# Performance work log

Hardware: AMD Instinct MI355X
Metric: run time of the kernel (lower is better)

The kernel has to match this reference:

```python
import jax, jax.numpy as jnp
import numpy as np
import math

B, T, D, DI, DFF, H = 4, 1024, 1024, 256, 4096, 16
S, N, E = 16, 256, 1024          # stat_num, token_num, exemplar_len
STAT_K, TOKEN_K = 8, 16
NEG = -1e6


def setup_inputs() -> dict:
    key = jax.random.key(0)
    ks = jax.random.split(key, 32)
    r = lambda i, shape: jax.random.normal(ks[i], shape, jnp.float32)
    w = lambda i, shape: r(i, shape) * 0.02
    return dict(
        x=r(0, (B, T, D)),
        stat_enc=r(1, (B * S, N, D)),
        exemplar_enc=r(2, (B, E, D)),
        stat_feature=r(3, (B, S, D)),
        intent_embed=r(4, (B, 1, DI)),
        Wq1=w(5, (D, D)), Wk1=w(6, (D, D)), Wv1=w(7, (D, D)), Wo1=w(8, (D, D)),
        Wq_stat=w(9, (D + DI, D)), Wq_token=w(10, (D + DI, D)),
        Wk_stat=w(11, (D, D)), Wk_token=w(12, (D, D)),
        Wv_sel=w(13, (D, D)), Wo_sel=w(14, (D, D)),
        Wq2=w(15, (D + DI, D)), Wk2=w(16, (D, D)), Wv2=w(17, (D, D)), Wo2=w(18, (D, D)),
        Wg=w(19, (2 * D, 1)),
        W1=w(20, (D, DFF)), b1=jnp.zeros((DFF,), jnp.float32),
        W2=w(21, (DFF, D)), b2=jnp.zeros((D,), jnp.float32),
        g1=jnp.ones((D,), jnp.float32), be1=jnp.zeros((D,), jnp.float32),
        g2=jnp.ones((D,), jnp.float32), be2=jnp.zeros((D,), jnp.float32),
        g3=jnp.ones((D,), jnp.float32), be3=jnp.zeros((D,), jnp.float32),
        stat_valid_len=jax.random.randint(ks[22], (B,), 1, S + 1),
        example_valid_len=jax.random.randint(ks[23], (B,), 1, E + 1),
    )


def _ln(x, g, b):
    m = x.mean(-1, keepdims=True)
    v = ((x - m) ** 2).mean(-1, keepdims=True)
    return (x - m) / jnp.sqrt(v + 1e-5) * g + b


def _mha(q, k, v, valid, Wq, Wk, Wv, Wo):
    Bq, Tq, _ = q.shape
    Sk = k.shape[1]
    sp = lambda z: z.reshape(Bq, z.shape[1], H, -1).transpose(0, 2, 1, 3)  # B,H,L,dh
    qh, kh, vh = sp(q @ Wq), sp(k @ Wk), sp(v @ Wv)
    dh = qh.shape[-1]
    sc = jnp.einsum('bhtd,bhsd->bhts', qh, kh) / math.sqrt(dh)
    vl = valid[:, None, None, None] if valid.ndim == 1 else valid[:, None, :, None]
    sc = jnp.where(jnp.arange(Sk)[None, None, None, :] < vl, sc, NEG)
    w = jax.nn.softmax(sc, axis=-1)
    out = jnp.einsum('bhts,bhsd->bhtd', w, vh).transpose(0, 2, 1, 3).reshape(Bq, Tq, -1)
    return out @ Wo


def _scatter_topk(scores, k):
    # keep top-k per row, everything else -> NEG (matches torch topk+scatter)
    shp = scores.shape
    flat = scores.reshape(-1, shp[-1])
    vals, idx = jax.lax.top_k(flat, k)
    out = jnp.full_like(flat, NEG).at[jnp.arange(flat.shape[0])[:, None], idx].set(vals)
    return out.reshape(shp)


def reference(x, stat_enc, exemplar_enc, stat_feature, intent_embed,
              Wq1, Wk1, Wv1, Wo1,
              Wq_stat, Wq_token, Wk_stat, Wk_token, Wv_sel, Wo_sel,
              Wq2, Wk2, Wv2, Wo2, Wg,
              W1, b1, W2, b2,
              g1, be1, g2, be2, g3, be3,
              stat_valid_len, example_valid_len):
    # masked self-attention (training mode -> causal valid lens)
    dec_valid = jnp.broadcast_to(jnp.arange(1, T + 1)[None, :], (B, T))
    x2 = _mha(x, x, x, dec_valid, Wq1, Wk1, Wv1, Wo1)
    y = _ln(x + x2, g1, be1)
    yi = jnp.concatenate([y, jnp.broadcast_to(intent_embed, (B, T, DI))], axis=-1)

    # selective hierarchical top-k attention
    qs = yi @ Wq_stat                      # [B,T,D]
    qt = yi @ Wq_token                     # [B,T,D]
    ks = stat_feature @ Wk_stat            # [B,S,D]
    kt = (stat_enc @ Wk_token).reshape(B, S, N, D)
    vv = (stat_enc @ Wv_sel).reshape(B, S, N, D)
    scale = math.sqrt(D)
    ssc = jnp.einsum('btd,bsd->bts', qs, ks) / scale
    ssc = jnp.where(jnp.arange(S)[None, None, :] < stat_valid_len[:, None, None], ssc, NEG)
    sw = jax.nn.softmax(_scatter_topk(ssc, min(S - 1, STAT_K)), axis=-1)   # [B,T,S]
    tsc = jnp.einsum('btd,bsnd->btsn', qt, kt) / scale                      # [B,T,S,N]
    tw = jax.nn.softmax(_scatter_topk(tsc, min(N - 1, TOKEN_K)), axis=-1)
    comb = sw[..., None] * tw                                               # [B,T,S,N]
    y2s = jnp.einsum('btsn,bsnd->btd', comb, vv) @ Wo_sel

    # exemplar cross-attention
    y2e = _mha(yi, exemplar_enc, exemplar_enc, example_valid_len, Wq2, Wk2, Wv2, Wo2)

    gate = jax.nn.sigmoid(jnp.concatenate([y2s, y2e], axis=-1) @ Wg)
    y2 = gate * y2s + (1.0 - gate) * y2e
    z = _ln(y + 2.0 * y2, g2, be2)
    ffn = jax.nn.relu(z @ W1 + b1) @ W2 + b2
    return _ln(z + ffn, g3, be3)
```

## Files before the change

kernel.cpp:

```cpp
#include <hip/hip_runtime.h>

typedef unsigned short u16;
typedef short s16x8 __attribute__((ext_vector_type(8)));
typedef u16 u16x4 __attribute__((ext_vector_type(4)));
typedef float f32x4 __attribute__((ext_vector_type(4)));

#define T_N   1024
#define NEGV  -1e6f
#define MB    (1L << 20)

__device__ __forceinline__ u16 f2bf(float f) {
    unsigned u = __float_as_uint(f);
    u += 0x7fffu + ((u >> 16) & 1u);
    return (u16)(u >> 16);
}
__device__ __forceinline__ float bf2f(u16 h) {
    return __uint_as_float(((unsigned)h) << 16);
}
__device__ __forceinline__ f32x4 mfma16(s16x8 a, s16x8 b, f32x4 c) {
    return __builtin_amdgcn_mfma_f32_16x16x32_bf16(a, b, c, 0, 0, 0);
}
__device__ __forceinline__ void gll16(const u16* g, u16* l) {
    __builtin_amdgcn_global_load_lds((const __attribute__((address_space(1))) void*)g,
                                     (__attribute__((address_space(3))) void*)l, 16, 0, 0);
}

struct P6 { const float* s[6]; u16* d[6]; };

__global__ __launch_bounds__(256) void transpose_cast_batch(P6 pp, int K, int N) {
    const float* __restrict__ src = pp.s[blockIdx.z];
    u16* __restrict__ dst = pp.d[blockIdx.z];
    __shared__ float tile[32][33];
    int nb = blockIdx.x * 32, kb = blockIdx.y * 32;
    int tx = threadIdx.x & 31, ty = threadIdx.x >> 5;
    #pragma unroll
    for (int i = 0; i < 4; i++)
        tile[ty + 8*i][tx] = src[(long)(kb + ty + 8*i) * N + nb + tx];
    __syncthreads();
    #pragma unroll
    for (int i = 0; i < 4; i++)
        dst[(long)(nb + ty + 8*i) * K + kb + tx] = f2bf(tile[tx][ty + 8*i]);
}

__global__ __launch_bounds__(256) void cast_bf16_kernel(const float* __restrict__ src,
                                                        u16* __restrict__ dst, long n) {
    long i = ((long)blockIdx.x * 256 + threadIdx.x) * 4;
    if (i >= n) return;
    float4 v = *(const float4*)(src + i);
    u16x4 o = { f2bf(v.x), f2bf(v.y), f2bf(v.z), f2bf(v.w) };
    *(u16x4*)(dst + i) = o;
}

template<typename OutT, bool RELU, bool HAS_BIAS>
__global__ __launch_bounds__(256) void gemm_bt(
    const u16* __restrict__ A, const u16* __restrict__ Bt, OutT* __restrict__ C,
    const float* __restrict__ bias, int M, int N, int K,
    int lda, int ldb, int ldc,
    int batchDivA, long sA, long sB, long sC)
{
    A  += (long)(blockIdx.z / batchDivA) * sA;
    Bt += (long)blockIdx.z * sB;
    C  += (long)blockIdx.z * sC;
    __shared__ __align__(16) u16 As[4096];
    __shared__ __align__(16) u16 Bs[4096];
    const int tid = threadIdx.x;
    const int wave = tid >> 6, lane = tid & 63;
    const int quad = lane >> 4, l16 = lane & 15;
    const int wr = (wave >> 1) * 64, wc = (wave & 1) * 64;
    const long row0 = (long)blockIdx.y * 128, col0 = (long)blockIdx.x * 128;

    f32x4 acc[4][4] = {};

    const int l4r = lane >> 2;
    const int l4c = (lane & 3) * 8;
    const int ra = wave * 32 + l4r;
    const u16* Ap0 = A + (row0 + ra) * (long)lda + l4c;
    const u16* Ap1 = Ap0 + 16L * lda;
    const u16* Bp0 = Bt + (col0 + ra) * (long)ldb + l4c;
    const u16* Bp1 = Bp0 + 16L * ldb;
    u16* AsW0 = &As[(wave * 32) * 32];
    u16* AsW1 = &As[(wave * 32 + 16) * 32];
    u16* BsW0 = &Bs[(wave * 32) * 32];
    u16* BsW1 = &Bs[(wave * 32 + 16) * 32];
    const bool aok0 = (row0 + wave * 32) < M;
    const bool aok1 = (row0 + wave * 32 + 16) < M;

    for (int k0 = 0; k0 < K; k0 += 32) {
        __syncthreads();
        if (aok0) gll16(Ap0 + k0, AsW0);
        if (aok1) gll16(Ap1 + k0, AsW1);
        gll16(Bp0 + k0, BsW0);
        gll16(Bp1 + k0, BsW1);
        __syncthreads();
        s16x8 af[4], bfr[4];
        #pragma unroll
        for (int i = 0; i < 4; i++)
            af[i]  = *(const s16x8*)&As[(wr + i*16 + l16) * 32 + quad*8];
        #pragma unroll
        for (int j = 0; j < 4; j++)
            bfr[j] = *(const s16x8*)&Bs[(wc + j*16 + l16) * 32 + quad*8];
        #pragma unroll
        for (int i = 0; i < 4; i++)
            #pragma unroll
            for (int j = 0; j < 4; j++)
                acc[i][j] = mfma16(af[i], bfr[j], acc[i][j]);
    }

    #pragma unroll
    for (int i = 0; i < 4; i++) {
        long row = row0 + wr + i*16 + quad*4;
        #pragma unroll
        for (int j = 0; j < 4; j++) {
            long col = col0 + wc + j*16 + l16;
            float bv = 0.f;
            if constexpr (HAS_BIAS) bv = bias[col];
            #pragma unroll
            for (int r = 0; r < 4; r++) {
                if (row + r < M) {
                    float v = acc[i][j][r] + bv;
                    if constexpr (RELU) v = fmaxf(v, 0.f);
                    if constexpr (sizeof(OutT) == 2) C[(row + r) * (long)ldc + col] = f2bf(v);
                    else                             C[(row + r) * (long)ldc + col] = v;
                }
            }
        }
    }
}

template<typename OutT, bool RELU, bool HAS_BIAS>
__global__ __launch_bounds__(512, 2) void gemm_bt256(
    const u16* __restrict__ A, const u16* __restrict__ Bt, OutT* __restrict__ C,
    const float* __restrict__ bias, int M, int N, int K,
    int lda, int ldb, int ldc,
    int batchDivA, long sA, long sB, long sC)
{
    A  += (long)(blockIdx.z / batchDivA) * sA;
    Bt += (long)blockIdx.z * sB;
    C  += (long)blockIdx.z * sC;
    __shared__ __align__(16) u16 As[4][8192];
    __shared__ __align__(16) u16 Bs[4][8192];
    const int tid = threadIdx.x;
    const int wave = tid >> 6, lane = tid & 63;
    const int quad = lane >> 4, l16 = lane & 15;
    const int wm = wave >> 2, wn = wave & 3;
    const long row0 = (long)blockIdx.y * 256, col0 = (long)blockIdx.x * 256;

    const int srow = tid >> 2;
    const int scol = ((tid & 3) ^ ((srow >> 1) & 3)) * 8;
    const u16* Ag = A  + (row0 + srow) * (long)lda + scol;
    const u16* Bg = Bt + (col0 + srow) * (long)ldb + scol;
    const int ldsoff = wave * 512;

    f32x4 acc[8][4] = {};
    const int NT = K >> 5;

    auto stageA = [&](int kt, int buf) {
        gll16(Ag + (long)kt * 32,            &As[buf][ldsoff]);
        gll16(Ag + (long)kt * 32 + 128L*lda, &As[buf][4096 + ldsoff]);
    };
    auto stageB = [&](int kt, int buf) {
        gll16(Bg + (long)kt * 32,            &Bs[buf][ldsoff]);
        gll16(Bg + (long)kt * 32 + 128L*ldb, &Bs[buf][4096 + ldsoff]);
    };

    stageA(0, 0); stageB(0, 0);
    stageA(1, 1); stageB(1, 1);
    stageA(2, 2); stageB(2, 2);
    asm volatile("s_waitcnt vmcnt(8)" ::: "memory");
    __builtin_amdgcn_s_barrier();

    const int arow = wm * 128 + l16;
    const int brow = wn * 64  + l16;
    const int kq   = (quad ^ ((l16 >> 1) & 3)) * 8;

    for (int kt = 0; kt < NT; ++kt) {
        const int b  = kt & 3;
        const int sb = (kt + 3) & 3;
        const bool st = (kt + 3) < NT;
        const u16* Ab = As[b];
        const u16* Bb = Bs[b];

        s16x8 bfr[4], af[4];
        #pragma unroll
        for (int j = 0; j < 4; ++j)
            bfr[j] = *(const s16x8*)&Bb[(brow + j*16) * 32 + kq];
        #pragma unroll
        for (int i = 0; i < 4; ++i)
            af[i] = *(const s16x8*)&Ab[(arow + i*16) * 32 + kq];
        if (st) stageA(kt + 3, sb);
        __builtin_amdgcn_s_barrier();
        asm volatile("s_waitcnt lgkmcnt(0)" ::: "memory");
        __builtin_amdgcn_sched_barrier(0);
        __builtin_amdgcn_s_setprio(1);
        #pragma unroll
        for (int i = 0; i < 4; ++i)
            #pragma unroll
            for (int j = 0; j < 4; ++j)
                acc[i][j] = mfma16(af[i], bfr[j], acc[i][j]);
        __builtin_amdgcn_s_setprio(0);
        __builtin_amdgcn_s_barrier();

        #pragma unroll
        for (int i = 0; i < 4; ++i)
            af[i] = *(const s16x8*)&Ab[(arow + (i + 4)*16) * 32 + kq];
        if (st) stageB(kt + 3, sb);
        __builtin_amdgcn_s_barrier();
        asm volatile("s_waitcnt lgkmcnt(0)" ::: "memory");
        __builtin_amdgcn_sched_barrier(0);
        __builtin_amdgcn_s_setprio(1);
        #pragma unroll
        for (int i = 0; i < 4; ++i)
            #pragma unroll
            for (int j = 0; j < 4; ++j)
                acc[i + 4][j] = mfma16(af[i], bfr[j], acc[i + 4][j]);
        __builtin_amdgcn_s_setprio(0);

        const int rem = NT - 2 - kt;
        if (rem >= 2)      asm volatile("s_waitcnt vmcnt(8)" ::: "memory");
        else if (rem == 1) asm volatile("s_waitcnt vmcnt(4)" ::: "memory");
        else if (rem == 0) asm volatile("s_waitcnt vmcnt(0)" ::: "memory");
        __builtin_amdgcn_s_barrier();
    }

    #pragma unroll
    for (int i = 0; i < 8; ++i) {
        const long row = row0 + wm*128 + i*16 + quad*4;
        #pragma unroll
        for (int j = 0; j < 4; ++j) {
            const long col = col0 + wn*64 + j*16 + l16;
            float bv = 0.f;
            if constexpr (HAS_BIAS) bv = bias[col];
            #pragma unroll
            for (int r = 0; r < 4; ++r) {
                float v = acc[i][j][r] + bv;
                if constexpr (RELU) v = fmaxf(v, 0.f);
                if constexpr (sizeof(OutT) == 2) C[(row + r) * (long)ldc + col] = f2bf(v);
                else                             C[(row + r) * (long)ldc + col] = v;
            }
        }
    }
}

template<bool CAUSAL>
__global__ __launch_bounds__(256) void flash_attn_kernel(
    const u16* __restrict__ Q, const u16* __restrict__ Kg, const u16* __restrict__ Vg,
    const int* __restrict__ valid_len, u16* __restrict__ O,
    int qld, int kld, int vld)
{
    const int h = blockIdx.y, b = blockIdx.z;
    const int qt0 = blockIdx.x * 64;
    const int tid = threadIdx.x;
    const int wave = tid >> 6, lane = tid & 63;
    const int quad = lane >> 4, l16 = lane & 15;

    __shared__ __align__(16) u16 Qs[64][72];
    __shared__ __align__(16) u16 Ks[64][72];
    __shared__ __align__(16) u16 Vt[64][72];
    __shared__ __align__(16) u16 Ps[4][16][72];

    const int sr = tid >> 2, scc = (tid & 3) * 16;
    {
        const u16* qp = Q + ((long)b * T_N + qt0 + sr) * qld + h * 64 + scc;
        *(s16x8*)&Qs[sr][scc]     = *(const s16x8*)qp;
        *(s16x8*)&Qs[sr][scc + 8] = *(const s16x8*)(qp + 8);
    }
    float m_i[4] = {-1e30f, -1e30f, -1e30f, -1e30f};
    float l_i[4] = {0.f, 0.f, 0.f, 0.f};
    f32x4 o_acc[4] = {};

    int vl = 0, kend;
    if (CAUSAL) kend = qt0 + 64;
    else { vl = valid_len[b]; kend = (vl + 63) & ~63; }

    for (int kv0 = 0; kv0 < kend; kv0 += 64) {
        __syncthreads();
        {
            const u16* kp = Kg + ((long)b * T_N + kv0 + sr) * kld + h * 64 + scc;
            *(s16x8*)&Ks[sr][scc]     = *(const s16x8*)kp;
            *(s16x8*)&Ks[sr][scc + 8] = *(const s16x8*)(kp + 8);
            const u16* vp = Vg + ((long)b * T_N + kv0 + sr) * vld + h * 64 + scc;
            s16x8 v0 = *(const s16x8*)vp;
            s16x8 v1 = *(const s16x8*)(vp + 8);
            #pragma unroll
            for (int j = 0; j < 8; j++) {
                Vt[scc + j][sr]     = (u16)v0[j];
                Vt[scc + 8 + j][sr] = (u16)v1[j];
            }
        }
        __syncthreads();
        f32x4 sc[4] = {};
        #pragma unroll
        for (int kk = 0; kk < 64; kk += 32) {
            s16x8 aq = *(const s16x8*)&Qs[wave*16 + l16][kk + quad*8];
            #pragma unroll
            for (int j = 0; j < 4; j++) {
                s16x8 bk = *(const s16x8*)&Ks[j*16 + l16][kk + quad*8];
                sc[j] = mfma16(aq, bk, sc[j]);
            }
        }
        const int qrow = qt0 + wave*16 + quad*4;
        #pragma unroll
        for (int j = 0; j < 4; j++) {
            int kcol = kv0 + j*16 + l16;
            #pragma unroll
            for (int r = 0; r < 4; r++) {
                float s = sc[j][r] * 0.125f;
                bool ok = CAUSAL ? (kcol <= qrow + r) : (kcol < vl);
                sc[j][r] = ok ? s : -1e30f;
            }
        }
        float alpha[4];
        #pragma unroll
        for (int r = 0; r < 4; r++) {
            float mx = fmaxf(fmaxf(sc[0][r], sc[1][r]), fmaxf(sc[2][r], sc[3][r]));
            #pragma unroll
            for (int d = 1; d < 16; d <<= 1) mx = fmaxf(mx, __shfl_xor(mx, d, 64));
            float mn = fmaxf(m_i[r], mx);
            alpha[r] = __expf(m_i[r] - mn);
            m_i[r] = mn;
        }
        float rsum[4] = {0.f, 0.f, 0.f, 0.f};
        #pragma unroll
        for (int j = 0; j < 4; j++)
            #pragma unroll
            for (int r = 0; r < 4; r++) {
                float pv = __expf(sc[j][r] - m_i[r]);
                sc[j][r] = pv;
                rsum[r] += pv;
            }
        #pragma unroll
        for (int r = 0; r < 4; r++) {
            #pragma unroll
            for (int d = 1; d < 16; d <<= 1) rsum[r] += __shfl_xor(rsum[r], d, 64);
            l_i[r] = l_i[r] * alpha[r] + rsum[r];
        }
        #pragma unroll
        for (int j = 0; j < 4; j++)
            #pragma unroll
            for (int r = 0; r < 4; r++)
                Ps[wave][quad*4 + r][j*16 + l16] = f2bf(sc[j][r]);
        #pragma unroll
        for (int j2 = 0; j2 < 4; j2++)
            #pragma unroll
            for (int r = 0; r < 4; r++)
                o_acc[j2][r] *= alpha[r];
        __syncthreads();
        #pragma unroll
        for (int kk = 0; kk < 64; kk += 32) {
            s16x8 ap = *(const s16x8*)&Ps[wave][l16][kk + quad*8];
            #pragma unroll
            for (int j2 = 0; j2 < 4; j2++) {
                s16x8 bv = *(const s16x8*)&Vt[j2*16 + l16][kk + quad*8];
                o_acc[j2] = mfma16(ap, bv, o_acc[j2]);
            }
        }
    }
    #pragma unroll
    for (int j2 = 0; j2 < 4; j2++) {
        #pragma unroll
        for (int r = 0; r < 4; r++) {
            float v = o_acc[j2][r] / l_i[r];
            long row = (long)b * T_N + qt0 + wave*16 + quad*4 + r;
            O[row * 1024 + h*64 + j2*16 + l16] = f2bf(v);
        }
    }
}

__global__ __launch_bounds__(256) void ssc_kernel(
    const u16* __restrict__ qs, const u16* __restrict__ ks,
    const int* __restrict__ svl, float* __restrict__ ssc, int qld)
{
    const int t = blockIdx.x, b = blockIdx.y;
    const int wave = threadIdx.x >> 6, lane = threadIdx.x & 63;
    const u16* qrow = qs + ((long)b * T_N + t) * qld + lane * 16;
    const int vl = svl[b];
    for (int s = wave; s < 16; s += 4) {
        const u16* krow = ks + ((long)b * 16 + s) * 1024 + lane * 16;
        float acc = 0.f;
        #pragma unroll
        for (int seg = 0; seg < 2; seg++) {
            s16x8 qv = *(const s16x8*)(qrow + seg*8);
            s16x8 kv = *(const s16x8*)(krow + seg*8);
            #pragma unroll
            for (int j = 0; j < 8; j++) acc += bf2f((u16)qv[j]) * bf2f((u16)kv[j]);
        }
        #pragma unroll
        for (int d = 1; d < 64; d <<= 1) acc += __shfl_xor(acc, d, 64);
        if (lane == 0)
            ssc[((long)b * T_N + t) * 16 + s] = (s < vl) ? acc * (1.f/32.f) : NEGV;
    }
}

__global__ __launch_bounds__(256) void select_combine_kernel(
    const float* __restrict__ ssc, const float* __restrict__ tsc,
    const u16* __restrict__ vv, u16* __restrict__ out, int t0, int vld)
{
    const int tl = blockIdx.x, b = blockIdx.y;
    const int tg = t0 + tl;
    const int tid = threadIdx.x;
    const int wave = tid >> 6, lane = tid & 63;
    __shared__ float coeff[128];
    __shared__ long  rowoff[128];
    __shared__ int   sel_s[8];
    __shared__ float sel_w[8];

    if (wave == 0) {
        float cur = (lane < 16) ? ssc[((long)b * T_N + tg) * 16 + lane] : -3e38f;
        float mx0 = 0.f, ssum = 0.f, myv = -3e38f;
        int myi = 0;
        #pragma unroll
        for (int it = 0; it < 8; it++) {
            float mv = cur; int mi = lane;
            #pragma unroll
            for (int d = 1; d < 64; d <<= 1) {
                float ov = __shfl_xor(mv, d, 64);
                int   oi = __shfl_xor(mi, d, 64);
                if (ov > mv || (ov == mv && oi < mi)) { mv = ov; mi = oi; }
            }
            if (it == 0) mx0 = mv;
            ssum += __expf(mv - mx0);
            if (lane == it) { myv = mv; myi = mi; }
            if (lane == mi) cur = -3e38f;
        }
        if (lane < 8) { sel_s[lane] = myi; sel_w[lane] = __expf(myv - mx0) / ssum; }
    }
    __syncthreads();

    for (int slot = wave; slot < 8; slot += 4) {
        int s = sel_s[slot];
        float sw = sel_w[slot];
        const float* trow = tsc + (((long)b * 16 + s) * 512 + tl) * 256;
        float4 lv4 = *(const float4*)(trow + lane * 4);
        float loc[4] = { lv4.x, lv4.y, lv4.z, lv4.w };
        float mx0 = 0.f, tsum = 0.f, myv = -3e38f;
        int myi = 0;
        for (int it = 0; it < 16; it++) {
            float mv = -3e38f; int mi = 0;
            #pragma unroll
            for (int u = 0; u < 4; u++)
                if (loc[u] > mv) { mv = loc[u]; mi = lane*4 + u; }
            #pragma unroll
            for (int d = 1; d < 64; d <<= 1) {
                float ov = __shfl_xor(mv, d, 64);
                int   oi = __shfl_xor(mi, d, 64);
                if (ov > mv || (ov == mv && oi < mi)) { mv = ov; mi = oi; }
            }
            if (it == 0) mx0 = mv * (1.f/32.f);
            tsum += __expf(mv * (1.f/32.f) - mx0);
            if (lane == it) { myv = mv; myi = mi; }
            if ((mi >> 2) == lane) {
                int u = mi & 3;
                if (u == 0) loc[0] = -3e38f;
                else if (u == 1) loc[1] = -3e38f;
                else if (u == 2) loc[2] = -3e38f;
                else loc[3] = -3e38f;
            }
        }
        if (lane < 16) {
            coeff[slot * 16 + lane]  = sw * __expf(myv * (1.f/32.f) - mx0) / tsum;
            rowoff[slot * 16 + lane] = (long)((b * 16 + s) * 256 + myi) * vld;
        }
    }
    __syncthreads();

    const int d0 = tid * 4;
    float a0 = 0.f, a1 = 0.f, a2 = 0.f, a3 = 0.f;
    for (int r = 0; r < 128; r++) {
        float c = coeff[r];
        const u16* vp = vv + rowoff[r] + d0;
        u16x4 v4 = *(const u16x4*)vp;
        a0 += c * bf2f(v4[0]);
        a1 += c * bf2f(v4[1]);
        a2 += c * bf2f(v4[2]);
        a3 += c * bf2f(v4[3]);
    }
    u16x4 o4 = { f2bf(a0), f2bf(a1), f2bf(a2), f2bf(a3) };
    *(u16x4*)(out + ((long)b * T_N + tg) * 1024 + d0) = o4;
}

__device__ __forceinline__ float block_sum(float v, float* red) {
    #pragma unroll
    for (int d = 1; d < 64; d <<= 1) v += __shfl_xor(v, d, 64);
    __syncthreads();
    if ((threadIdx.x & 63) == 0) red[threadIdx.x >> 6] = v;
    __syncthreads();
    return red[0] + red[1] + red[2] + red[3];
}

__global__ __launch_bounds__(256) void ln1_kernel(
    const float* __restrict__ x, const float* __restrict__ x2,
    const float* __restrict__ intent, const float* __restrict__ g, const float* __restrict__ be,
    u16* __restrict__ yi)
{
    __shared__ float red[4];
    const long row = blockIdx.x;
    const int tid = threadIdx.x;
    const long base = row * 1024 + tid * 4;
    float4 xv = *(const float4*)(x + base);
    float4 dv = *(const float4*)(x2 + base);
    float h0 = xv.x + dv.x, h1 = xv.y + dv.y, h2 = xv.z + dv.z, h3 = xv.w + dv.w;
    float s1 = block_sum(h0 + h1 + h2 + h3, red);
    float s2 = block_sum(h0*h0 + h1*h1 + h2*h2 + h3*h3, red);
    float mean = s1 * (1.f/1024.f);
    float var = s2 * (1.f/1024.f) - mean * mean;
    float inv = rsqrtf(var + 1e-5f);
    const int c = tid * 4;
    float4 gv = *(const float4*)(g + c);
    float4 bv = *(const float4*)(be + c);
    float o0 = (h0 - mean) * inv * gv.x + bv.x;
    float o1 = (h1 - mean) * inv * gv.y + bv.y;
    float o2 = (h2 - mean) * inv * gv.z + bv.z;
    float o3 = (h3 - mean) * inv * gv.w + bv.w;
    u16x4 ob = { f2bf(o0), f2bf(o1), f2bf(o2), f2bf(o3) };
    *(u16x4*)(yi + row * 1280 + c) = ob;
    const int b = (int)(row >> 10);
    yi[row * 1280 + 1024 + tid] = f2bf(intent[b * 256 + tid]);
}

__global__ __launch_bounds__(256) void gate_ln2_kernel(
    const u16* __restrict__ yi, const float* __restrict__ y2s, const float* __restrict__ y2e,
    const float* __restrict__ Wg, const float* __restrict__ g, const float* __restrict__ be,
    float* __restrict__ z, u16* __restrict__ zbf)
{
    __shared__ float red[4];
    const long row = blockIdx.x;
    const int tid = threadIdx.x;
    const long base = row * 1024 + tid * 4;
    const int c = tid * 4;
    float4 sv = *(const float4*)(y2s + base);
    float4 ev = *(const float4*)(y2e + base);
    float4 w1 = *(const float4*)(Wg + c);
    float4 w2 = *(const float4*)(Wg + 1024 + c);
    float dot = sv.x*w1.x + sv.y*w1.y + sv.z*w1.z + sv.w*w1.w
              + ev.x*w2.x + ev.y*w2.y + ev.z*w2.z + ev.w*w2.w;
    float tot = block_sum(dot, red);
    float gate = 1.f / (1.f + __expf(-tot));
    u16x4 yv4 = *(const u16x4*)(yi + row * 1280 + c);
    float h0 = bf2f(yv4[0]) + 2.f * (gate * sv.x + (1.f - gate) * ev.x);
    float h1 = bf2f(yv4[1]) + 2.f * (gate * sv.y + (1.f - gate) * ev.y);
    float h2 = bf2f(yv4[2]) + 2.f * (gate * sv.z + (1.f - gate) * ev.z);
    float h3 = bf2f(yv4[3]) + 2.f * (gate * sv.w + (1.f - gate) * ev.w);
    float s1 = block_sum(h0 + h1 + h2 + h3, red);
    float s2 = block_sum(h0*h0 + h1*h1 + h2*h2 + h3*h3, red);
    float mean = s1 * (1.f/1024.f);
    float var = s2 * (1.f/1024.f) - mean * mean;
    float inv = rsqrtf(var + 1e-5f);
    float4 gv = *(const float4*)(g + c);
    float4 bv = *(const float4*)(be + c);
    float o0 = (h0 - mean) * inv * gv.x + bv.x;
    float o1 = (h1 - mean) * inv * gv.y + bv.y;
    float o2 = (h2 - mean) * inv * gv.z + bv.z;
    float o3 = (h3 - mean) * inv * gv.w + bv.w;
    *(float4*)(z + base) = make_float4(o0, o1, o2, o3);
    u16x4 ob = { f2bf(o0), f2bf(o1), f2bf(o2), f2bf(o3) };
    *(u16x4*)(zbf + row * 1024 + c) = ob;
}

__global__ __launch_bounds__(256) void ln3_kernel(
    const float* __restrict__ z, const float* __restrict__ p0, const float* __restrict__ p1,
    const float* __restrict__ b2,
    const float* __restrict__ g, const float* __restrict__ be, float* __restrict__ out)
{
    __shared__ float red[4];
    const long row = blockIdx.x;
    const int tid = threadIdx.x;
    const long base = row * 1024 + tid * 4;
    const int c = tid * 4;
    float4 zv = *(const float4*)(z + base);
    float4 f0 = *(const float4*)(p0 + base);
    float4 f1 = *(const float4*)(p1 + base);
    float4 bb = *(const float4*)(b2 + c);
    float h0 = zv.x + f0.x + f1.x + bb.x;
    float h1 = zv.y + f0.y + f1.y + bb.y;
    float h2 = zv.z + f0.z + f1.z + bb.z;
    float h3 = zv.w + f0.w + f1.w + bb.w;
    float s1 = block_sum(h0 + h1 + h2 + h3, red);
    float s2 = block_sum(h0*h0 + h1*h1 + h2*h2 + h3*h3, red);
    float mean = s1 * (1.f/1024.f);
    float var = s2 * (1.f/1024.f) - mean * mean;
    float inv = rsqrtf(var + 1e-5f);
    float4 gv = *(const float4*)(g + c);
    float4 bv = *(const float4*)(be + c);
    float o0 = (h0 - mean) * inv * gv.x + bv.x;
    float o1 = (h1 - mean) * inv * gv.y + bv.y;
    float o2 = (h2 - mean) * inv * gv.z + bv.z;
    float o3 = (h3 - mean) * inv * gv.w + bv.w;
    *(float4*)(out + base) = make_float4(o0, o1, o2, o3);
}

extern "C" void kernel_launch(void* const* d_in, const int* in_sizes, int n_in,
                              void* d_out, int out_size, void* d_ws, size_t ws_size,
                              hipStream_t stream)
{
    (void)in_sizes; (void)n_in; (void)out_size; (void)ws_size;
    const float* x      = (const float*)d_in[0];
    const float* stat_e = (const float*)d_in[1];
    const float* exem   = (const float*)d_in[2];
    const float* sfeat  = (const float*)d_in[3];
    const float* intent = (const float*)d_in[4];
    const float* Wg  = (const float*)d_in[19];
    const float* b1  = (const float*)d_in[21];
    const float* b2  = (const float*)d_in[23];
    const float* g1  = (const float*)d_in[24]; const float* be1 = (const float*)d_in[25];
    const float* g2  = (const float*)d_in[26]; const float* be2 = (const float*)d_in[27];
    const float* g3  = (const float*)d_in[28]; const float* be3 = (const float*)d_in[29];
    const int* svl = (const int*)d_in[30];
    const int* evl = (const int*)d_in[31];
    float* outp = (float*)d_out;

    char* base = (char*)d_ws;
    u16*  bufA  = (u16*)(base + 0*MB);
    u16*  qkv1  = (u16*)(base + 8*MB);
    float* x2a  = (float*)(base + 8*MB);
    u16*  kv2   = (u16*)(base + 8*MB);
    u16*  w1t   = (u16*)(base + 8*MB);
    u16*  w2t   = (u16*)(base + 16*MB);
    u16*  yibf  = (u16*)(base + 32*MB);
    u16*  buf3  = (u16*)(base + 42*MB);
    u16*  zbf   = (u16*)(base + 42*MB);
    u16*  sebf  = (u16*)(base + 66*MB);
    float* tsch = (float*)(base + 66*MB);
    u16*  hid   = (u16*)(base + 66*MB);
    u16*  ktvv  = (u16*)(base + 98*MB);
    float* y2sf = (float*)(base + 98*MB);
    float* p0f  = (float*)(base + 98*MB);
    u16*  exbf  = (u16*)(base + 114*MB);
    float* y2ef = (float*)(base + 122*MB);
    float* zf   = (float*)(base + 138*MB);
    u16*  sfbf  = (u16*)(base + 162*MB);
    u16*  ksbf  = (u16*)(base + 162*MB + 256*1024);
    float* sscf = (float*)(base + 162*MB + 512*1024);
    char* wpool = base + 163*MB;

    dim3 blk(256);
    dim3 blk512(512);
    auto cast = [&](const float* s, u16* d, long n) {
        cast_bf16_kernel<<<dim3((unsigned)((n/4 + 255) / 256)), blk, 0, stream>>>(s, d, n);
    };
    auto g_n = [&](const u16* A, const u16* Bt, u16* C, int M, int N, int K,
                   int lda, int ldb, int ldc) {
        gemm_bt<u16,false,false><<<dim3(N/128, (M+127)/128, 1), blk, 0, stream>>>(
            A, Bt, C, nullptr, M, N, K, lda, ldb, ldc, 1, 0, 0, 0);
    };
    auto g_f = [&](const u16* A, const u16* Bt, float* C, int M, int N, int K,
                   int lda, int ldb, int ldc) {
        gemm_bt<float,false,false><<<dim3(N/128, (M+127)/128, 1), blk, 0, stream>>>(
            A, Bt, C, nullptr, M, N, K, lda, ldb, ldc, 1, 0, 0, 0);
    };
    auto g256_n = [&](const u16* A, const u16* Bt, u16* C, int M, int N, int K,
                      int lda, int ldb, int ldc) {
        gemm_bt256<u16,false,false><<<dim3(N/256, M/256, 1), blk512, 0, stream>>>(
            A, Bt, C, nullptr, M, N, K, lda, ldb, ldc, 1, 0, 0, 0);
    };

    u16* wqkv1t = (u16*)wpool;
    u16* wo1t   = (u16*)(wpool) + 3L*1024*1024;
    {
        P6 pp{};
        pp.s[0]=(const float*)d_in[5]; pp.d[0]=wqkv1t;
        pp.s[1]=(const float*)d_in[6]; pp.d[1]=wqkv1t + 1L*1024*1024;
        pp.s[2]=(const float*)d_in[7]; pp.d[2]=wqkv1t + 2L*1024*1024;
        pp.s[3]=(const float*)d_in[8]; pp.d[3]=wo1t;
        transpose_cast_batch<<<dim3(32, 32, 4), blk, 0, stream>>>(pp, 1024, 1024);
    }
    cast(x, bufA, 4096L*1024);
    g256_n(bufA, wqkv1t, qkv1, 4096, 3072, 1024, 1024, 1024, 3072);
    flash_attn_kernel<true><<<dim3(16, 16, 4), blk, 0, stream>>>(
        qkv1, qkv1 + 1024, qkv1 + 2048, nullptr, bufA, 3072, 3072, 3072);
    g_f(bufA, wo1t, x2a, 4096, 1024, 1024, 1024, 1024, 1024);
    ln1_kernel<<<dim3(4096), blk, 0, stream>>>(x, x2a, intent, g1, be1, yibf);

    u16* wq3t = (u16*)wpool;
    {
        P6 pp{};
        pp.s[0]=(const float*)d_in[9];  pp.d[0]=wq3t;
        pp.s[1]=(const float*)d_in[10]; pp.d[1]=wq3t + 1L*1024*1280;
        pp.s[2]=(const float*)d_in[15]; pp.d[2]=wq3t + 2L*1024*1280;
        transpose_cast_batch<<<dim3(32, 40, 3), blk, 0, stream>>>(pp, 1280, 1024);
    }
    g256_n(yibf, wq3t, buf3, 4096, 3072, 1280, 1280, 1280, 3072);
    u16* wkst = (u16*)wpool;
    u16* wkv  = (u16*)(wpool) + 1L*1024*1024;
    {
        P6 pp{};
        pp.s[0]=(const float*)d_in[11]; pp.d[0]=wkst;
        pp.s[1]=(const float*)d_in[12]; pp.d[1]=wkv;
        pp.s[2]=(const float*)d_in[13]; pp.d[2]=wkv + 1L*1024*1024;
        transpose_cast_batch<<<dim3(32, 32, 3), blk, 0, stream>>>(pp, 1024, 1024);
    }
    cast(sfeat, sfbf, 64L*1024);
    cast(stat_e, sebf, 16384L*1024);
    g_n(sfbf, wkst, ksbf, 64, 1024, 1024, 1024, 1024, 1024);
    g256_n(sebf, wkv, ktvv, 16384, 2048, 1024, 1024, 1024, 2048);
    ssc_kernel<<<dim3(1024, 4), blk, 0, stream>>>(buf3, ksbf, svl, sscf, 3072);
    for (int hh = 0; hh < 2; hh++) {
        long t0 = hh * 512;
        gemm_bt<float,false,false><<<dim3(2, 4, 64), blk, 0, stream>>>(
            buf3 + 1024 + t0*3072, ktvv, tsch, nullptr, 512, 256, 1024,
            3072, 2048, 256, 16, (long)T_N*3072, 256L*2048, 512L*256);
        select_combine_kernel<<<dim3(512, 4), blk, 0, stream>>>(
            sscf, tsch, ktvv + 1024, bufA, (int)t0, 2048);
    }
    u16* wost = (u16*)wpool;
    u16* wkv2 = (u16*)(wpool) + 1L*1024*1024;
    u16* wo2t = (u16*)(wpool) + 3L*1024*1024;
    {
        P6 pp{};
        pp.s[0]=(const float*)d_in[14]; pp.d[0]=wost;
        pp.s[1]=(const float*)d_in[16]; pp.d[1]=wkv2;
        pp.s[2]=(const float*)d_in[17]; pp.d[2]=wkv2 + 1L*1024*1024;
        pp.s[3]=(const float*)d_in[18]; pp.d[3]=wo2t;
        transpose_cast_batch<<<dim3(32, 32, 4), blk, 0, stream>>>(pp, 1024, 1024);
    }
    g_f(bufA, wost, y2sf, 4096, 1024, 1024, 1024, 1024, 1024);

    cast(exem, exbf, 4096L*1024);
    g_n(exbf, wkv2, kv2, 4096, 2048, 1024, 1024, 1024, 2048);
    flash_attn_kernel<false><<<dim3(16, 16, 4), blk, 0, stream>>>(
        buf3 + 2048, kv2, kv2 + 1024, evl, bufA, 3072, 2048, 2048);
    g_f(bufA, wo2t, y2ef, 4096, 1024, 1024, 1024, 1024, 1024);

    gate_ln2_kernel<<<dim3(4096), blk, 0, stream>>>(yibf, y2sf, y2ef, Wg, g2, be2, zf, zbf);

    {
        P6 pp{}; pp.s[0] = (const float*)d_in[20]; pp.d[0] = w1t;
        transpose_cast_batch<<<dim3(128, 32, 1), blk, 0, stream>>>(pp, 1024, 4096);
    }
    {
        P6 pp{}; pp.s[0] = (const float*)d_in[22]; pp.d[0] = w2t;
        transpose_cast_batch<<<dim3(32, 128, 1), blk, 0, stream>>>(pp, 4096, 1024);
    }
    gemm_bt256<u16,true,true><<<dim3(16, 16, 1), blk512, 0, stream>>>(
        zbf, w1t, hid, b1, 4096, 4096, 1024, 1024, 1024, 4096, 1, 0, 0, 0);
    gemm_bt<float,false,false><<<dim3(8, 32, 2), blk, 0, stream>>>(
        hid, w2t, p0f, nullptr, 4096, 1024, 2048, 4096, 4096, 1024,
        1, 2048, 2048, 4096L*1024);

    ln3_kernel<<<dim3(4096), blk, 0, stream>>>(zf, p0f, p0f + 4096L*1024, b2, g3, be3, outp);
}
```

Measured before the change: 1.018 ms.

## Remap GEMM tiles across XCDs and flatten the k-loop into one MFMA phase

Adds a workgroup-ID remap so that consecutive tiles land on the same XCD, which is meant to improve L2 reuse of A and B panels. It also collapses the two-phase k-loop (two barriers per phase, setprio, split A-fragment loads) into a single phase: all eight A fragments are loaded at once, A and B for step kt+3 are staged together, and 32 MFMAs are issued back to back with one barrier per iteration. This cuts barrier and synchronisation overhead but raises register pressure from holding eight A fragments, and it drops the explicit lgkmcnt wait and priority hints, leaving LDS-load ordering to the compiler.

```diff
diff --git a/kernel.cpp b/kernel.cpp
--- a/kernel.cpp
+++ b/kernel.cpp
@@ -134,6 +134,16 @@
     int lda, int ldb, int ldc,
     int batchDivA, long sA, long sB, long sC)
 {
+    int bx = blockIdx.x, by = blockIdx.y;
+    {
+        const int nwg = gridDim.x * gridDim.y;
+        if ((nwg & 7) == 0) {
+            const int flat = by * gridDim.x + bx;
+            const int nf = (flat & 7) * (nwg >> 3) + (flat >> 3);
+            bx = nf % gridDim.x;
+            by = nf / gridDim.x;
+        }
+    }
     A  += (long)(blockIdx.z / batchDivA) * sA;
     Bt += (long)blockIdx.z * sB;
     C  += (long)blockIdx.z * sC;
@@ -143,7 +153,7 @@
     const int wave = tid >> 6, lane = tid & 63;
     const int quad = lane >> 4, l16 = lane & 15;
     const int wm = wave >> 2, wn = wave & 3;
-    const long row0 = (long)blockIdx.y * 256, col0 = (long)blockIdx.x * 256;
+    const long row0 = (long)by * 256, col0 = (long)bx * 256;
 
     const int srow = tid >> 2;
     const int scol = ((tid & 3) ^ ((srow >> 1) & 3)) * 8;
@@ -168,6 +178,7 @@
     stageA(2, 2); stageB(2, 2);
     asm volatile("s_waitcnt vmcnt(8)" ::: "memory");
     __builtin_amdgcn_s_barrier();
+    __builtin_amdgcn_sched_barrier(0);
 
     const int arow = wm * 128 + l16;
     const int brow = wn * 64  + l16;
@@ -180,46 +191,28 @@
         const u16* Ab = As[b];
         const u16* Bb = Bs[b];
 
-        s16x8 bfr[4], af[4];
+        s16x8 bfr[4], af[8];
         #pragma unroll
         for (int j = 0; j < 4; ++j)
             bfr[j] = *(const s16x8*)&Bb[(brow + j*16) * 32 + kq];
         #pragma unroll
-        for (int i = 0; i < 4; ++i)
+        for (int i = 0; i < 8; ++i)
             af[i] = *(const s16x8*)&Ab[(arow + i*16) * 32 + kq];
-        if (st) stageA(kt + 3, sb);
-        __builtin_amdgcn_s_barrier();
-        asm volatile("s_waitcnt lgkmcnt(0)" ::: "memory");
-        __builtin_amdgcn_sched_barrier(0);
-        __builtin_amdgcn_s_setprio(1);
-        #pragma unroll
-        for (int i = 0; i < 4; ++i)
+
+        if (st) { stageA(kt + 3, sb); stageB(kt + 3, sb); }
+
+        #pragma unroll
+        for (int i = 0; i < 8; ++i)
             #pragma unroll
             for (int j = 0; j < 4; ++j)
                 acc[i][j] = mfma16(af[i], bfr[j], acc[i][j]);
-        __builtin_amdgcn_s_setprio(0);
-        __builtin_amdgcn_s_barrier();
-
-        #pragma unroll
-        for (int i = 0; i < 4; ++i)
-            af[i] = *(const s16x8*)&Ab[(arow + (i + 4)*16) * 32 + kq];
-        if (st) stageB(kt + 3, sb);
-        __builtin_amdgcn_s_barrier();
-        asm volatile("s_waitcnt lgkmcnt(0)" ::: "memory");
-        __builtin_amdgcn_sched_barrier(0);
-        __builtin_amdgcn_s_setprio(1);
-        #pragma unroll
-        for (int i = 0; i < 4; ++i)
-            #pragma unroll
-            for (int j = 0; j < 4; ++j)
-                acc[i + 4][j] = mfma16(af[i], bfr[j], acc[i + 4][j]);
-        __builtin_amdgcn_s_setprio(0);
 
         const int rem = NT - 2 - kt;
         if (rem >= 2)      asm volatile("s_waitcnt vmcnt(8)" ::: "memory");
         else if (rem == 1) asm volatile("s_waitcnt vmcnt(4)" ::: "memory");
         else if (rem == 0) asm volatile("s_waitcnt vmcnt(0)" ::: "memory");
         __builtin_amdgcn_s_barrier();
+        __builtin_amdgcn_sched_barrier(0);
     }
 
     #pragma unroll
```

Measured after the change: 1.005 ms. About the same (-1.3%).
